# Kernel optimization log

Measured on AMD Instinct MI355X. Metric: run time of the kernel, lower is better.

The kernel has to match this reference:

```python
import jax, jax.numpy as jnp
import numpy as np

HIDDEN = 1024
N_HEADS = 16
D_HEAD = HIDDEN // N_HEADS
B, S = 4, 2048


def setup_inputs() -> dict:
    key = jax.random.key(0)
    ks = jax.random.split(key, 7)
    scale = 1.0 / np.sqrt(D_HEAD)
    return {
        "sequences": jax.random.normal(ks[0], (B, S, HIDDEN), dtype=jnp.float32),
        "Wq": jax.random.normal(ks[1], (N_HEADS, D_HEAD, D_HEAD), dtype=jnp.float32) * scale,
        "bq": jax.random.normal(ks[2], (N_HEADS, D_HEAD), dtype=jnp.float32) * 0.02,
        "Wk": jax.random.normal(ks[3], (N_HEADS, D_HEAD, D_HEAD), dtype=jnp.float32) * scale,
        "bk": jax.random.normal(ks[4], (N_HEADS, D_HEAD), dtype=jnp.float32) * 0.02,
        "Wv": jax.random.normal(ks[5], (N_HEADS, D_HEAD, D_HEAD), dtype=jnp.float32) * scale,
        "bv": jax.random.normal(ks[6], (N_HEADS, D_HEAD), dtype=jnp.float32) * 0.02,
    }


def reference(sequences, Wq, bq, Wk, bk, Wv, bv):
    # sequences: [B, S, hidden]; split hidden into per-head slices -> [B, S, H, d]
    x = sequences.reshape(B, S, N_HEADS, D_HEAD)
    # per-head Linear: y = x @ W^T + b (torch nn.Linear convention)
    q = jnp.einsum("bshd,hed->bshe", x, Wq) + bq  # [B,S,H,d]
    k = jnp.einsum("bshd,hed->bshe", x, Wk) + bk
    v = jnp.einsum("bshd,hed->bshe", x, Wv) + bv
    scores = jnp.einsum("bqhd,bkhd->bhqk", q, k) / np.sqrt(D_HEAD)  # [B,H,S,S]
    attn = jax.nn.softmax(scores, axis=-1)
    out = jnp.einsum("bhqk,bkhd->bqhd", attn, v)  # [B,S,H,d]
    # hstack over heads == concat along feature dim
    return out.reshape(B, S, HIDDEN)
```

## Files before the change

kernel.cpp:

```cpp
#include <hip/hip_runtime.h>
#include <hip/hip_bf16.h>

#define NB 4
#define NS 2048
#define NH 16
#define ND 64
#define NHID 1024
#define NT (NS / 64)
#define QSCALE 0.18033688011112042f

typedef __bf16 bf16x8 __attribute__((ext_vector_type(8)));
typedef _Float16 f16x8 __attribute__((ext_vector_type(8)));
typedef _Float16 f16x4 __attribute__((ext_vector_type(4)));
typedef __fp16 h16x2 __attribute__((ext_vector_type(2)));
typedef float f32x4 __attribute__((ext_vector_type(4)));

#define GLDS16(g, l)                                                      \
  __builtin_amdgcn_global_load_lds(                                       \
      (const __attribute__((address_space(1))) void*)(g),                 \
      (__attribute__((address_space(3))) void*)(l), 16, 0, 0)

__device__ __forceinline__ bf16x8 cvt8(const float* __restrict__ p) {
  float4 f0 = *(const float4*)p;
  float4 f1 = *(const float4*)(p + 4);
  bf16x8 v;
  v[0] = (__bf16)f0.x; v[1] = (__bf16)f0.y; v[2] = (__bf16)f0.z; v[3] = (__bf16)f0.w;
  v[4] = (__bf16)f1.x; v[5] = (__bf16)f1.y; v[6] = (__bf16)f1.z; v[7] = (__bf16)f1.w;
  return v;
}

__global__ void wcvt(const float* __restrict__ Wq, const float* __restrict__ Wk,
                     const float* __restrict__ Wv, __bf16* __restrict__ Wb) {
  const int M = NH * ND * ND;
  int i = blockIdx.x * 256 + threadIdx.x;
  float v;
  if (i < M)            v = Wq[i] * QSCALE;
  else if (i < 2 * M)   v = Wk[i - M];
  else                  v = Wv[i - 2 * M];
  Wb[i] = (__bf16)v;
}

__global__ __launch_bounds__(256, 2) void qkv_proj(
    const float* __restrict__ x, const __bf16* __restrict__ Wb,
    const float* __restrict__ bq, const float* __restrict__ bk,
    const float* __restrict__ bv,
    __bf16* __restrict__ qs, __bf16* __restrict__ ks, _Float16* __restrict__ vt)
{
  __shared__ __align__(16) unsigned short tiles[4][64 * 72];

  const int bid = blockIdx.x;
  const int hg = bid & 3;
  const int s0 = ((bid >> 2) & 31) * 64;
  const int b  = bid >> 7;
  const int tid  = threadIdx.x;
  const int w    = tid >> 6;
  const int lane = tid & 63;
  const int l16  = lane & 15;
  const int quad = lane >> 4;
  const int h  = hg * 4 + w;
  const int bh = b * NH + h;

  unsigned short* tile = tiles[w];
  __bf16*   tb16 = (__bf16*)tile;
  _Float16* tf16 = (_Float16*)tile;

  bf16x8 aX[4][2];
#pragma unroll
  for (int tb = 0; tb < 4; ++tb) {
    const float* xrow = x + ((size_t)(b * NS + s0 + tb * 16 + l16)) * NHID + h * ND;
#pragma unroll
    for (int k2 = 0; k2 < 2; ++k2)
      aX[tb][k2] = cvt8(xrow + k2 * 32 + quad * 8);
  }

#pragma unroll
  for (int mat = 0; mat < 3; ++mat) {
    const __bf16* Wm = Wb + ((size_t)(mat * NH + h)) * ND * ND;
    const float* bm = (mat == 0) ? bq : (mat == 1) ? bk : bv;

    f32x4 acc[4][4];
#pragma unroll
    for (int nb = 0; nb < 4; ++nb) {
      const int e = nb * 16 + l16;
      bf16x8 w0 = *(const bf16x8*)(Wm + e * ND + quad * 8);
      bf16x8 w1 = *(const bf16x8*)(Wm + e * ND + 32 + quad * 8);
#pragma unroll
      for (int tbk = 0; tbk < 4; ++tbk) {
        f32x4 a = {0.f, 0.f, 0.f, 0.f};
        a = __builtin_amdgcn_mfma_f32_16x16x32_bf16(aX[tbk][0], w0, a, 0, 0, 0);
        a = __builtin_amdgcn_mfma_f32_16x16x32_bf16(aX[tbk][1], w1, a, 0, 0, 0);
        acc[nb][tbk] = a;
      }
    }

    if (mat < 2) {
#pragma unroll
      for (int nb = 0; nb < 4; ++nb) {
        float bias = bm[h * ND + nb * 16 + l16] * ((mat == 0) ? QSCALE : 1.0f);
#pragma unroll
        for (int tbk = 0; tbk < 4; ++tbk)
#pragma unroll
          for (int r = 0; r < 4; ++r)
            tb16[(tbk * 16 + quad * 4 + r) * 72 + nb * 16 + l16] =
                (__bf16)(acc[nb][tbk][r] + bias);
      }
#pragma unroll
      for (int p = 0; p < 8; ++p) {
        int idx = p * 64 + lane, row = idx >> 3, c = idx & 7;
        bf16x8 v8 = *(const bf16x8*)(tb16 + row * 72 + c * 8);
        if (mat == 0)
          *(bf16x8*)(qs + ((size_t)bh * NS + s0 + row) * ND + c * 8) = v8;
        else
          *(bf16x8*)(ks + ((size_t)bh * NS + s0 + row) * ND + ((c ^ (row & 7)) * 8)) = v8;
      }
    } else {
#pragma unroll
      for (int nb = 0; nb < 4; ++nb) {
        float bias = bm[h * ND + nb * 16 + l16];
#pragma unroll
        for (int tbk = 0; tbk < 4; ++tbk) {
          union { h16x2 h2[2]; uint2 u2; } pv;
          pv.h2[0] = __builtin_amdgcn_cvt_pkrtz(acc[nb][tbk][0] + bias,
                                                acc[nb][tbk][1] + bias);
          pv.h2[1] = __builtin_amdgcn_cvt_pkrtz(acc[nb][tbk][2] + bias,
                                                acc[nb][tbk][3] + bias);
          *(uint2*)&tf16[(nb * 16 + l16) * 72 + tbk * 16 + quad * 4] = pv.u2;
        }
      }
#pragma unroll
      for (int p = 0; p < 8; ++p) {
        int idx = p * 64 + lane, row = idx >> 3, c = idx & 7;
        int K0 = 32 * (c >> 2) + 4 * (c & 3);
        union { f16x4 v4[2]; f16x8 v8; } u;
        u.v4[0] = *(const f16x4*)(tf16 + row * 72 + K0);
        u.v4[1] = *(const f16x4*)(tf16 + row * 72 + K0 + 16);
        *(f16x8*)(vt + ((size_t)bh * ND + row) * NS + s0 + ((c ^ (row & 7)) * 8)) = u.v8;
      }
    }
  }
}

__global__ __launch_bounds__(256, 2) void attn(
    const __bf16* __restrict__ qs, const __bf16* __restrict__ ks,
    const _Float16* __restrict__ vt, float* __restrict__ out)
{
  __shared__ __align__(16) __bf16   KT[2][64 * 64];
  __shared__ __align__(16) _Float16 VT[2][64 * 64];

  const int bid = blockIdx.x;
  const int qt = bid >> 6;
  const int h  = bid & 15;
  const int b  = (bid >> 4) & 3;
  const int bh = b * NH + h;
  const int tid  = threadIdx.x;
  const int w    = tid >> 6;
  const int lane = tid & 63;
  const int l16  = lane & 15;
  const int quad = lane >> 4;
  const int swz  = l16 & 7;
  const int qw   = qt * 256 + w * 64;

  const __bf16*   Kb = ks + (size_t)bh * NS * ND;
  const _Float16* Vb = vt + (size_t)bh * ND * NS;

  bf16x8 Qf[4][2];
#pragma unroll
  for (int qb = 0; qb < 4; ++qb)
#pragma unroll
    for (int k2 = 0; k2 < 2; ++k2)
      Qf[qb][k2] = *(const bf16x8*)(qs + ((size_t)bh * NS + qw + qb * 16 + l16) * ND +
                                    k2 * 32 + quad * 8);

  f32x4 acc[4][4];
#pragma unroll
  for (int qb = 0; qb < 4; ++qb)
#pragma unroll
    for (int mb = 0; mb < 4; ++mb) acc[qb][mb] = (f32x4){0.f, 0.f, 0.f, 0.f};
  float lp[4] = {0.f, 0.f, 0.f, 0.f};

#pragma unroll
  for (int p = 0; p < 2; ++p) {
    int i = (w * 2 + p) * 64 + lane;
    GLDS16(Kb + (size_t)0 * 4096 + i * 8, &KT[0][i * 8]);
    int row = i >> 3, cc = i & 7;
    GLDS16(Vb + (size_t)row * NS + 0 * 64 + cc * 8, &VT[0][i * 8]);
  }

  for (int kt = 0; kt < NT; ++kt) {
    const int cur = kt & 1;
    __syncthreads();
    if (kt + 1 < NT) {
      const int nxt = cur ^ 1;
#pragma unroll
      for (int p = 0; p < 2; ++p) {
        int i = (w * 2 + p) * 64 + lane;
        GLDS16(Kb + (size_t)(kt + 1) * 4096 + i * 8, &KT[nxt][i * 8]);
        int row = i >> 3, cc = i & 7;
        GLDS16(Vb + (size_t)row * NS + (kt + 1) * 64 + cc * 8, &VT[nxt][i * 8]);
      }
    }

    const __bf16*   Kl = KT[cur];
    const _Float16* Vl = VT[cur];

    f32x4 sc[4][4];
#pragma unroll
    for (int kb = 0; kb < 4; ++kb) {
      const __bf16* krow = Kl + (kb * 16 + l16) * 64;
      bf16x8 Kf0 = *(const bf16x8*)(krow + ((quad ^ swz) * 8));
      bf16x8 Kf1 = *(const bf16x8*)(krow + (((4 + quad) ^ swz) * 8));
#pragma unroll
      for (int qb = 0; qb < 4; ++qb) {
        f32x4 s = {0.f, 0.f, 0.f, 0.f};
        s = __builtin_amdgcn_mfma_f32_16x16x32_bf16(Kf0, Qf[qb][0], s, 0, 0, 0);
        s = __builtin_amdgcn_mfma_f32_16x16x32_bf16(Kf1, Qf[qb][1], s, 0, 0, 0);
        sc[qb][kb] = s;
      }
    }

    f16x8 bp8[4][2];
#pragma unroll
    for (int qb = 0; qb < 4; ++qb) {
#pragma unroll
      for (int g = 0; g < 2; ++g) {
        float p0 = __builtin_amdgcn_exp2f(sc[qb][2 * g][0]);
        float p1 = __builtin_amdgcn_exp2f(sc[qb][2 * g][1]);
        float p2 = __builtin_amdgcn_exp2f(sc[qb][2 * g][2]);
        float p3 = __builtin_amdgcn_exp2f(sc[qb][2 * g][3]);
        float p4 = __builtin_amdgcn_exp2f(sc[qb][2 * g + 1][0]);
        float p5 = __builtin_amdgcn_exp2f(sc[qb][2 * g + 1][1]);
        float p6 = __builtin_amdgcn_exp2f(sc[qb][2 * g + 1][2]);
        float p7 = __builtin_amdgcn_exp2f(sc[qb][2 * g + 1][3]);
        lp[qb] += ((p0 + p1) + (p2 + p3)) + ((p4 + p5) + (p6 + p7));
        union { h16x2 v2[4]; f16x8 v8; } u;
        u.v2[0] = __builtin_amdgcn_cvt_pkrtz(p0, p1);
        u.v2[1] = __builtin_amdgcn_cvt_pkrtz(p2, p3);
        u.v2[2] = __builtin_amdgcn_cvt_pkrtz(p4, p5);
        u.v2[3] = __builtin_amdgcn_cvt_pkrtz(p6, p7);
        bp8[qb][g] = u.v8;
      }
    }

#pragma unroll
    for (int g = 0; g < 2; ++g) {
#pragma unroll
      for (int mb = 0; mb < 4; ++mb) {
        f16x8 Vf = *(const f16x8*)(Vl + (mb * 16 + l16) * 64 + (((g * 4 + quad) ^ swz)) * 8);
#pragma unroll
        for (int qb = 0; qb < 4; ++qb)
          acc[qb][mb] = __builtin_amdgcn_mfma_f32_16x16x32_f16(Vf, bp8[qb][g], acc[qb][mb], 0, 0, 0);
      }
    }
  }

#pragma unroll
  for (int qb = 0; qb < 4; ++qb) {
    float ls = lp[qb];
    ls += __shfl_xor(ls, 16, 64);
    ls += __shfl_xor(ls, 32, 64);
    float invl = 1.0f / ls;
    const size_t orow = ((size_t)(b * NS) + qw + qb * 16 + l16) * NHID + h * ND;
#pragma unroll
    for (int mb = 0; mb < 4; ++mb) {
      float4 o4 = {acc[qb][mb][0] * invl, acc[qb][mb][1] * invl,
                   acc[qb][mb][2] * invl, acc[qb][mb][3] * invl};
      *(float4*)(out + orow + mb * 16 + quad * 4) = o4;
    }
  }
}

extern "C" void kernel_launch(void* const* d_in, const int* in_sizes, int n_in,
                              void* d_out, int out_size, void* d_ws, size_t ws_size,
                              hipStream_t stream) {
  const float* x  = (const float*)d_in[0];
  const float* Wq = (const float*)d_in[1];
  const float* bq = (const float*)d_in[2];
  const float* Wk = (const float*)d_in[3];
  const float* bk = (const float*)d_in[4];
  const float* Wv = (const float*)d_in[5];
  const float* bv = (const float*)d_in[6];
  float* out = (float*)d_out;

  const size_t per = (size_t)NB * NH * NS * ND;
  __bf16* qs   = (__bf16*)d_ws;
  __bf16* ksb  = qs + per;
  _Float16* vt = (_Float16*)(ksb + per);
  __bf16* Wb   = (__bf16*)(vt + per);

  wcvt<<<768, 256, 0, stream>>>(Wq, Wk, Wv, Wb);
  qkv_proj<<<NB * (NS / 64) * (NH / 4), 256, 0, stream>>>(x, Wb, bq, bk, bv, qs, ksb, vt);
  attn<<<8 * NB * NH, 256, 0, stream>>>(qs, ksb, vt, out);
}
```

Baseline: 174.2 us.

## Fuse weight conversion into projection, compute softmax row sums via MFMA, add setprio

Removes the separate weight-conversion kernel: the projection kernel now reads fp32 weights and converts them to bf16 with scaling inline, which saves one launch and a workspace round trip. In the attention kernel, the scalar per-lane accumulation of softmax denominators and the final cross-lane shuffles are replaced by an extra MFMA against a ones vector, which moves that work onto the matrix units. s_setprio is also raised around the MFMA sections to favour matrix issue across waves. The trade-offs are redundant weight conversion in every projection block, extra MFMA work per tile, and the row sum now being accumulated from fp16-rounded probabilities.

After: 172.4 us (median of 2 runs). Within noise of the previous version (-1.0%).

```diff
diff --git a/kernel.cpp b/kernel.cpp
--- a/kernel.cpp
+++ b/kernel.cpp
@@ -29,19 +29,21 @@
   return v;
 }
 
-__global__ void wcvt(const float* __restrict__ Wq, const float* __restrict__ Wk,
-                     const float* __restrict__ Wv, __bf16* __restrict__ Wb) {
-  const int M = NH * ND * ND;
-  int i = blockIdx.x * 256 + threadIdx.x;
-  float v;
-  if (i < M)            v = Wq[i] * QSCALE;
-  else if (i < 2 * M)   v = Wk[i - M];
-  else                  v = Wv[i - 2 * M];
-  Wb[i] = (__bf16)v;
+__device__ __forceinline__ bf16x8 cvt8s(const float* __restrict__ p, float s) {
+  float4 f0 = *(const float4*)p;
+  float4 f1 = *(const float4*)(p + 4);
+  bf16x8 v;
+  v[0] = (__bf16)(f0.x * s); v[1] = (__bf16)(f0.y * s);
+  v[2] = (__bf16)(f0.z * s); v[3] = (__bf16)(f0.w * s);
+  v[4] = (__bf16)(f1.x * s); v[5] = (__bf16)(f1.y * s);
+  v[6] = (__bf16)(f1.z * s); v[7] = (__bf16)(f1.w * s);
+  return v;
 }
 
 __global__ __launch_bounds__(256, 2) void qkv_proj(
-    const float* __restrict__ x, const __bf16* __restrict__ Wb,
+    const float* __restrict__ x,
+    const float* __restrict__ Wq, const float* __restrict__ Wk,
+    const float* __restrict__ Wv,
     const float* __restrict__ bq, const float* __restrict__ bk,
     const float* __restrict__ bv,
     __bf16* __restrict__ qs, __bf16* __restrict__ ks, _Float16* __restrict__ vt)
@@ -75,15 +77,16 @@
 
 #pragma unroll
   for (int mat = 0; mat < 3; ++mat) {
-    const __bf16* Wm = Wb + ((size_t)(mat * NH + h)) * ND * ND;
+    const float* Wm = ((mat == 0) ? Wq : (mat == 1) ? Wk : Wv) + (size_t)h * ND * ND;
     const float* bm = (mat == 0) ? bq : (mat == 1) ? bk : bv;
+    const float wsc = (mat == 0) ? QSCALE : 1.0f;
 
     f32x4 acc[4][4];
 #pragma unroll
     for (int nb = 0; nb < 4; ++nb) {
       const int e = nb * 16 + l16;
-      bf16x8 w0 = *(const bf16x8*)(Wm + e * ND + quad * 8);
-      bf16x8 w1 = *(const bf16x8*)(Wm + e * ND + 32 + quad * 8);
+      bf16x8 w0 = cvt8s(Wm + e * ND + quad * 8, wsc);
+      bf16x8 w1 = cvt8s(Wm + e * ND + 32 + quad * 8, wsc);
 #pragma unroll
       for (int tbk = 0; tbk < 4; ++tbk) {
         f32x4 a = {0.f, 0.f, 0.f, 0.f};
@@ -96,7 +99,7 @@
     if (mat < 2) {
 #pragma unroll
       for (int nb = 0; nb < 4; ++nb) {
-        float bias = bm[h * ND + nb * 16 + l16] * ((mat == 0) ? QSCALE : 1.0f);
+        float bias = bm[h * ND + nb * 16 + l16] * wsc;
 #pragma unroll
         for (int tbk = 0; tbk < 4; ++tbk)
 #pragma unroll
@@ -176,7 +179,11 @@
   for (int qb = 0; qb < 4; ++qb)
 #pragma unroll
     for (int mb = 0; mb < 4; ++mb) acc[qb][mb] = (f32x4){0.f, 0.f, 0.f, 0.f};
-  float lp[4] = {0.f, 0.f, 0.f, 0.f};
+  f32x4 lacc[4];
+#pragma unroll
+  for (int qb = 0; qb < 4; ++qb) lacc[qb] = (f32x4){0.f, 0.f, 0.f, 0.f};
+  const f16x8 onesf = {(_Float16)1.f, (_Float16)1.f, (_Float16)1.f, (_Float16)1.f,
+                       (_Float16)1.f, (_Float16)1.f, (_Float16)1.f, (_Float16)1.f};
 
 #pragma unroll
   for (int p = 0; p < 2; ++p) {
@@ -204,6 +211,7 @@
     const _Float16* Vl = VT[cur];
 
     f32x4 sc[4][4];
+    __builtin_amdgcn_s_setprio(1);
 #pragma unroll
     for (int kb = 0; kb < 4; ++kb) {
       const __bf16* krow = Kl + (kb * 16 + l16) * 64;
@@ -217,6 +225,7 @@
         sc[qb][kb] = s;
       }
     }
+    __builtin_amdgcn_s_setprio(0);
 
     f16x8 bp8[4][2];
 #pragma unroll
@@ -231,7 +240,6 @@
         float p5 = __builtin_amdgcn_exp2f(sc[qb][2 * g + 1][1]);
         float p6 = __builtin_amdgcn_exp2f(sc[qb][2 * g + 1][2]);
         float p7 = __builtin_amdgcn_exp2f(sc[qb][2 * g + 1][3]);
-        lp[qb] += ((p0 + p1) + (p2 + p3)) + ((p4 + p5) + (p6 + p7));
         union { h16x2 v2[4]; f16x8 v8; } u;
         u.v2[0] = __builtin_amdgcn_cvt_pkrtz(p0, p1);
         u.v2[1] = __builtin_amdgcn_cvt_pkrtz(p2, p3);
@@ -241,6 +249,7 @@
       }
     }
 
+    __builtin_amdgcn_s_setprio(1);
 #pragma unroll
     for (int g = 0; g < 2; ++g) {
 #pragma unroll
@@ -250,15 +259,16 @@
         for (int qb = 0; qb < 4; ++qb)
           acc[qb][mb] = __builtin_amdgcn_mfma_f32_16x16x32_f16(Vf, bp8[qb][g], acc[qb][mb], 0, 0, 0);
       }
-    }
+#pragma unroll
+      for (int qb = 0; qb < 4; ++qb)
+        lacc[qb] = __builtin_amdgcn_mfma_f32_16x16x32_f16(onesf, bp8[qb][g], lacc[qb], 0, 0, 0);
+    }
+    __builtin_amdgcn_s_setprio(0);
   }
 
 #pragma unroll
   for (int qb = 0; qb < 4; ++qb) {
-    float ls = lp[qb];
-    ls += __shfl_xor(ls, 16, 64);
-    ls += __shfl_xor(ls, 32, 64);
-    float invl = 1.0f / ls;
+    float invl = 1.0f / lacc[qb][0];
     const size_t orow = ((size_t)(b * NS) + qw + qb * 16 + l16) * NHID + h * ND;
 #pragma unroll
     for (int mb = 0; mb < 4; ++mb) {
@@ -285,9 +295,8 @@
   __bf16* qs   = (__bf16*)d_ws;
   __bf16* ksb  = qs + per;
   _Float16* vt = (_Float16*)(ksb + per);
-  __bf16* Wb   = (__bf16*)(vt + per);
-
-  wcvt<<<768, 256, 0, stream>>>(Wq, Wk, Wv, Wb);
-  qkv_proj<<<NB * (NS / 64) * (NH / 4), 256, 0, stream>>>(x, Wb, bq, bk, bv, qs, ksb, vt);
+
+  qkv_proj<<<NB * (NS / 64) * (NH / 4), 256, 0, stream>>>(
+      x, Wq, Wk, Wv, bq, bk, bv, qs, ksb, vt);
   attn<<<8 * NB * NH, 256, 0, stream>>>(qs, ksb, vt, out);
 }
```
